# Optimization experiments

Measured on AMD Instinct MI355X. Metric: run time of the kernel, lower is better.

## Reference

```python
import jax, jax.numpy as jnp
import numpy as np

B, N, E, D = 1, 50000, 800000, 128


def _mlp(x, w1, b1, w2, b2, w3, b3):
    # MLP(in, hidden, out, l=2): Linear+ReLU, Linear+ReLU, Linear
    h = jax.nn.relu(x @ w1 + b1)
    h = jax.nn.relu(h @ w2 + b2)
    return h @ w3 + b3


def _glorot(key, shape):
    fan_in, fan_out = shape[0], shape[1]
    lim = np.sqrt(6.0 / (fan_in + fan_out)).astype(np.float32)
    return jax.random.uniform(key, shape, jnp.float32, -lim, lim)


def setup_inputs() -> dict:
    key = jax.random.key(0)
    ks = jax.random.split(key, 16)
    inp = {
        "nodes": jax.random.normal(ks[0], (B, N, D), jnp.float32),
        "senders": jax.random.randint(ks[1], (E,), 0, N, jnp.int32),
        "receivers": jax.random.randint(ks[2], (E,), 0, N, jnp.int32),
        # message MLP params: 2D -> D -> D -> D
        "mw1": _glorot(ks[3], (2 * D, D)), "mb1": jnp.zeros((D,), jnp.float32),
        "mw2": _glorot(ks[4], (D, D)),     "mb2": jnp.zeros((D,), jnp.float32),
        "mw3": _glorot(ks[5], (D, D)),     "mb3": jnp.zeros((D,), jnp.float32),
        # node MLP params: 2D -> D -> D -> D
        "nw1": _glorot(ks[6], (2 * D, D)), "nb1": jnp.zeros((D,), jnp.float32),
        "nw2": _glorot(ks[7], (D, D)),     "nb2": jnp.zeros((D,), jnp.float32),
        "nw3": _glorot(ks[8], (D, D)),     "nb3": jnp.zeros((D,), jnp.float32),
    }
    return inp


def reference(nodes, senders, receivers,
              mw1, mb1, mw2, mb2, mw3, mb3,
              nw1, nb1, nw2, nb2, nw3, nb3):
    # gather endpoint features: [B, E, 2D]
    edge_in = jnp.concatenate((nodes[:, receivers], nodes[:, senders]), axis=-1)
    messages = _mlp(edge_in, mw1, mb1, mw2, mb2, mw3, mb3)  # [B, E, D]
    # scatter-add messages into receiver inbox: [B, N, D]
    inbox = jnp.zeros_like(nodes).at[:, receivers].add(messages)
    node_in = jnp.concatenate((nodes, inbox), axis=-1)  # [B, N, 2D]
    return nodes + _mlp(node_in, nw1, nb1, nw2, nb2, nw3, nb3)
```

## Files before the change

### kernel.cpp

```cpp
#include <hip/hip_runtime.h>
#include <hip/hip_bf16.h>
#include <stdint.h>

typedef __bf16 bf16;
typedef bf16 bf16x8 __attribute__((ext_vector_type(8)));
typedef float f32x4 __attribute__((ext_vector_type(4)));

#define N_NODES 50000
#define FEAT 128
#define NB_SCAN ((N_NODES + 1023) / 1024)

static constexpr size_t UV_BYTES    = (size_t)N_NODES * 256 * 2;
static constexpr size_t INBOX_BYTES = (size_t)N_NODES * FEAT * 4;

#define WUV_OFF 0
#define WM2_OFF 32768
#define WM3_OFF 49152
#define WN1_OFF 65536
#define WN2_OFF 98304
#define WN3_OFF 114688
#define W_TOTAL 131072
static constexpr size_t W_BYTES = (size_t)W_TOTAL * 2;

__device__ __forceinline__ bf16x8 cvt_f32x8_bf16(const float* __restrict__ p) {
  float4 f0 = *(const float4*)p;
  float4 f1 = *(const float4*)(p + 4);
  bf16x8 t;
  t[0] = (bf16)f0.x; t[1] = (bf16)f0.y; t[2] = (bf16)f0.z; t[3] = (bf16)f0.w;
  t[4] = (bf16)f1.x; t[5] = (bf16)f1.y; t[6] = (bf16)f1.z; t[7] = (bf16)f1.w;
  return t;
}

__global__ void prep_weights_kernel(const float* __restrict__ mw1, const float* __restrict__ mw2,
                                    const float* __restrict__ mw3, const float* __restrict__ nw1,
                                    const float* __restrict__ nw2, const float* __restrict__ nw3,
                                    bf16* __restrict__ w) {
  int i = blockIdx.x * blockDim.x + threadIdx.x;
  if (i >= W_TOTAL) return;
  float v;
  if (i < WM2_OFF) {
    int c = i >> 7, k = i & 127;
    v = (c < 128) ? mw1[k * 128 + c] : mw1[(128 + k) * 128 + (c - 128)];
  } else if (i < WM3_OFF) {
    int j = i - WM2_OFF; int c = j >> 7, k = j & 127;
    v = mw2[k * 128 + c];
  } else if (i < WN1_OFF) {
    int j = i - WM3_OFF; int c = j >> 7, k = j & 127;
    v = mw3[k * 128 + c];
  } else if (i < WN2_OFF) {
    int j = i - WN1_OFF; int c = j >> 8, k = j & 255;
    v = nw1[k * 128 + c];
  } else if (i < WN3_OFF) {
    int j = i - WN2_OFF; int c = j >> 7, k = j & 127;
    v = nw2[k * 128 + c];
  } else {
    int j = i - WN3_OFF; int c = j >> 7, k = j & 127;
    v = nw3[k * 128 + c];
  }
  w[i] = (bf16)v;
}

__global__ void hist_kernel(const int* __restrict__ receivers, int* __restrict__ cnt, int E) {
  int i = blockIdx.x * blockDim.x + threadIdx.x;
  if (i < E) atomicAdd(&cnt[receivers[i]], 1);
}

__global__ __launch_bounds__(1024) void scan1_kernel(const int* __restrict__ cnt,
                                                     int* __restrict__ offs,
                                                     int* __restrict__ bsum) {
  __shared__ int s[1024];
  const int tid = threadIdx.x;
  const int g = blockIdx.x * 1024 + tid;
  int x = (g < N_NODES) ? cnt[g] : 0;
  s[tid] = x;
  __syncthreads();
  for (int off = 1; off < 1024; off <<= 1) {
    int v = (tid >= off) ? s[tid - off] : 0;
    __syncthreads();
    s[tid] += v;
    __syncthreads();
  }
  if (g < N_NODES) offs[g] = s[tid] - x;
  if (tid == 1023) bsum[blockIdx.x] = s[tid];
}

__global__ void scan2_kernel(int* __restrict__ bsum) {
  __shared__ int s[64];
  const int tid = threadIdx.x;
  int x = (tid < NB_SCAN) ? bsum[tid] : 0;
  s[tid] = x;
  __syncthreads();
  for (int off = 1; off < 64; off <<= 1) {
    int v = (tid >= off) ? s[tid - off] : 0;
    __syncthreads();
    s[tid] += v;
    __syncthreads();
  }
  if (tid < NB_SCAN) bsum[tid] = s[tid] - x;
}

__global__ __launch_bounds__(1024) void scan3_kernel(int* __restrict__ offs,
                                                     const int* __restrict__ bsum, int E) {
  const int tid = threadIdx.x;
  const int g = blockIdx.x * 1024 + tid;
  if (g < N_NODES) offs[g] += bsum[blockIdx.x];
  if (blockIdx.x == 0 && tid == 0) offs[N_NODES] = E;
}

__global__ void scatter_ids_kernel(const int* __restrict__ senders,
                                   const int* __restrict__ receivers,
                                   const int* __restrict__ offs, int* __restrict__ cur,
                                   int* __restrict__ sSend, int* __restrict__ sRecv, int E) {
  int i = blockIdx.x * blockDim.x + threadIdx.x;
  if (i < E) {
    int r = receivers[i];
    int slot = offs[r] + atomicAdd(&cur[r], 1);
    sSend[slot] = senders[i];
    sRecv[slot] = r;
  }
}

__global__ __launch_bounds__(512) void uv_gemm_kernel(const float* __restrict__ nodes,
                                                      const bf16* __restrict__ wuvt,
                                                      const float* __restrict__ mb1,
                                                      bf16* __restrict__ uv) {
  const int tid = threadIdx.x;
  const int lane = tid & 63, wid = tid >> 6;
  const int wm = wid >> 2, wn = wid & 3;
  const int rBase = blockIdx.x * 128 + wm * 64;
  const int cBase = wn * 64;
  const int l15 = lane & 15, ka = (lane >> 4) * 8, rj = (lane >> 4) * 4;

  f32x4 acc[4][4];
#pragma unroll
  for (int mi = 0; mi < 4; ++mi)
#pragma unroll
    for (int ni = 0; ni < 4; ++ni) acc[mi][ni] = (f32x4){0.f, 0.f, 0.f, 0.f};

#pragma unroll
  for (int kk = 0; kk < 4; ++kk) {
    const int k0 = kk * 32 + ka;
    bf16x8 a[4], b[4];
#pragma unroll
    for (int mi = 0; mi < 4; ++mi) {
      int r = rBase + mi * 16 + l15;
      if (r > N_NODES - 1) r = N_NODES - 1;
      a[mi] = cvt_f32x8_bf16(nodes + (size_t)r * FEAT + k0);
    }
#pragma unroll
    for (int ni = 0; ni < 4; ++ni) {
      int c = cBase + ni * 16 + l15;
      b[ni] = *(const bf16x8*)(wuvt + (size_t)c * 128 + k0);
    }
#pragma unroll
    for (int mi = 0; mi < 4; ++mi)
#pragma unroll
      for (int ni = 0; ni < 4; ++ni)
        acc[mi][ni] = __builtin_amdgcn_mfma_f32_16x16x32_bf16(a[mi], b[ni], acc[mi][ni], 0, 0, 0);
  }
#pragma unroll
  for (int mi = 0; mi < 4; ++mi)
#pragma unroll
    for (int ni = 0; ni < 4; ++ni) {
      int c = cBase + ni * 16 + l15;
      float bias = (c < FEAT) ? mb1[c] : 0.f;
#pragma unroll
      for (int j = 0; j < 4; ++j) {
        int r = rBase + mi * 16 + rj + j;
        if (r < N_NODES) uv[(size_t)r * 256 + c] = (bf16)(acc[mi][ni][j] + bias);
      }
    }
}

#define EB 128
__global__ __launch_bounds__(256, 3) void edge_kernel(const bf16* __restrict__ uv,
                                                      const int* __restrict__ sSend,
                                                      const int* __restrict__ sRecv,
                                                      const bf16* __restrict__ wm2t,
                                                      const bf16* __restrict__ wm3t,
                                                      const float* __restrict__ mb2,
                                                      const float* __restrict__ mb3,
                                                      float* __restrict__ inbox, int E) {
  __shared__ int rIds[EB];
  __shared__ int sIds[EB];
  __shared__ bf16 hbuf[4][32 * 128];

  const int tid = threadIdx.x;
  const int e0 = blockIdx.x * EB;
  const int rMax = (E - e0 < EB) ? (E - e0) : EB;

  if (tid < EB) {
    int e = e0 + tid; if (e >= E) e = E - 1;
    rIds[tid] = sRecv[e];
  } else {
    int t = tid - EB;
    int e = e0 + t; if (e >= E) e = E - 1;
    sIds[t] = sSend[e];
  }
  __syncthreads();

  const int lane = tid & 63, wid = tid >> 6;
  const int l15 = lane & 15, ka = (lane >> 4) * 8, rj = (lane >> 4) * 4;
  const int rW = wid * 32;
  bf16* hw = hbuf[wid];

  bf16x8 afr[2][4];
#pragma unroll
  for (int mi = 0; mi < 2; ++mi) {
    int row = rW + mi * 16 + l15;
    int recv = rIds[row], send = sIds[row];
    const bf16* up = uv + (size_t)recv * 256;
    const bf16* vp = uv + (size_t)send * 256 + 128;
#pragma unroll
    for (int kk = 0; kk < 4; ++kk) {
      int k0 = kk * 32 + ka;
      bf16x8 u8 = *(const bf16x8*)(up + k0);
      bf16x8 v8 = *(const bf16x8*)(vp + k0);
      bf16x8 h;
#pragma unroll
      for (int t = 0; t < 8; ++t) {
        float x = (float)u8[t] + (float)v8[t];
        h[t] = (bf16)(x > 0.f ? x : 0.f);
      }
      afr[mi][kk] = h;
    }
  }

  f32x4 acc[2][8];
#pragma unroll
  for (int mi = 0; mi < 2; ++mi)
#pragma unroll
    for (int ni = 0; ni < 8; ++ni) acc[mi][ni] = (f32x4){0.f, 0.f, 0.f, 0.f};
#pragma unroll
  for (int kk = 0; kk < 4; ++kk) {
    const int k0 = kk * 32 + ka;
    bf16x8 b[8];
#pragma unroll
    for (int ni = 0; ni < 8; ++ni) {
      int c = ni * 16 + l15;
      b[ni] = *(const bf16x8*)(wm2t + (size_t)c * 128 + k0);
    }
#pragma unroll
    for (int mi = 0; mi < 2; ++mi)
#pragma unroll
      for (int ni = 0; ni < 8; ++ni)
        acc[mi][ni] = __builtin_amdgcn_mfma_f32_16x16x32_bf16(afr[mi][kk], b[ni], acc[mi][ni], 0, 0, 0);
  }

#pragma unroll
  for (int mi = 0; mi < 2; ++mi)
#pragma unroll
    for (int ni = 0; ni < 8; ++ni) {
      int c = ni * 16 + l15;
      float bias = mb2[c];
#pragma unroll
      for (int j = 0; j < 4; ++j) {
        int row = mi * 16 + rj + j;
        float v = acc[mi][ni][j] + bias;
        v = v > 0.f ? v : 0.f;
        int byte = row * 256 + ((c * 2) ^ ((row & 7) << 4));
        *(bf16*)((char*)hw + byte) = (bf16)v;
      }
    }
  asm volatile("s_waitcnt lgkmcnt(0)" ::: "memory");
  __builtin_amdgcn_sched_barrier(0);

  bf16x8 a3[2][4];
#pragma unroll
  for (int mi = 0; mi < 2; ++mi) {
    int row = mi * 16 + l15;
#pragma unroll
    for (int kk = 0; kk < 4; ++kk) {
      int k0 = kk * 32 + ka;
      int byte = row * 256 + ((k0 * 2) ^ ((row & 7) << 4));
      a3[mi][kk] = *(const bf16x8*)((const char*)hw + byte);
    }
  }
  f32x4 acc3[2][8];
#pragma unroll
  for (int mi = 0; mi < 2; ++mi)
#pragma unroll
    for (int ni = 0; ni < 8; ++ni) acc3[mi][ni] = (f32x4){0.f, 0.f, 0.f, 0.f};
#pragma unroll
  for (int kk = 0; kk < 4; ++kk) {
    const int k0 = kk * 32 + ka;
    bf16x8 b[8];
#pragma unroll
    for (int ni = 0; ni < 8; ++ni) {
      int c = ni * 16 + l15;
      b[ni] = *(const bf16x8*)(wm3t + (size_t)c * 128 + k0);
    }
#pragma unroll
    for (int mi = 0; mi < 2; ++mi)
#pragma unroll
      for (int ni = 0; ni < 8; ++ni)
        acc3[mi][ni] = __builtin_amdgcn_mfma_f32_16x16x32_bf16(a3[mi][kk], b[ni], acc3[mi][ni], 0, 0, 0);
  }

  asm volatile("s_waitcnt lgkmcnt(0)" ::: "memory");
  __builtin_amdgcn_sched_barrier(0);
#pragma unroll
  for (int mi = 0; mi < 2; ++mi)
#pragma unroll
    for (int ni = 0; ni < 8; ++ni) {
      int c = ni * 16 + l15;
      float bias = mb3[c];
#pragma unroll
      for (int j = 0; j < 4; ++j) {
        int row = mi * 16 + rj + j;
        int byte = row * 256 + ((c * 2) ^ ((row & 7) << 4));
        *(bf16*)((char*)hw + byte) = (bf16)(acc3[mi][ni][j] + bias);
      }
    }
  asm volatile("s_waitcnt lgkmcnt(0)" ::: "memory");
  __builtin_amdgcn_sched_barrier(0);

  uint32_t pr[32];
#pragma unroll
  for (int r = 0; r < 32; ++r) {
    int byte = r * 256 + ((4 * lane) ^ ((r & 7) << 4));
    pr[r] = *(const uint32_t*)((const char*)hw + byte);
  }
  const int cb = 2 * lane;
  float s0 = 0.f, s1 = 0.f;
#pragma unroll
  for (int r = 0; r < 32; ++r) {
    int grow = rW + r;
    if (grow >= rMax) break;
    s0 += __uint_as_float(pr[r] << 16);
    s1 += __uint_as_float(pr[r] & 0xffff0000u);
    int recv = rIds[grow];
    bool flush = (r == 31) || (grow + 1 >= rMax) || (rIds[grow + 1] != recv);
    if (flush) {
      float* dst = inbox + (size_t)recv * FEAT + cb;
      unsafeAtomicAdd(dst, s0);
      unsafeAtomicAdd(dst + 1, s1);
      s0 = 0.f; s1 = 0.f;
    }
  }
}

__global__ __launch_bounds__(512) void node_kernel(const float* __restrict__ nodes,
                                                   const float* __restrict__ inbox,
                                                   const bf16* __restrict__ wn1t,
                                                   const bf16* __restrict__ wn2t,
                                                   const bf16* __restrict__ wn3t,
                                                   const float* __restrict__ nb1,
                                                   const float* __restrict__ nb2,
                                                   const float* __restrict__ nb3,
                                                   float* __restrict__ out) {
  __shared__ bf16 h1[256 * 128];
  __shared__ bf16 h2[256 * 128];
  const int tid = threadIdx.x;
  const int lane = tid & 63, wid = tid >> 6;
  const int wm = wid >> 1, wn = wid & 1;
  const int rBase = wm * 64, cBase = wn * 64;
  const int l15 = lane & 15, ka = (lane >> 4) * 8, rj = (lane >> 4) * 4;
  const int nBase = blockIdx.x * 256;

  f32x4 acc[4][4];
#pragma unroll
  for (int mi = 0; mi < 4; ++mi)
#pragma unroll
    for (int ni = 0; ni < 4; ++ni) acc[mi][ni] = (f32x4){0.f, 0.f, 0.f, 0.f};
#pragma unroll
  for (int kk = 0; kk < 8; ++kk) {
    const int k0 = kk * 32 + ka;
    bf16x8 a[4], b[4];
#pragma unroll
    for (int mi = 0; mi < 4; ++mi) {
      int n = nBase + rBase + mi * 16 + l15;
      if (n > N_NODES - 1) n = N_NODES - 1;
      const float* src = (kk < 4) ? (nodes + (size_t)n * FEAT + k0)
                                  : (inbox + (size_t)n * FEAT + (k0 - 128));
      a[mi] = cvt_f32x8_bf16(src);
    }
#pragma unroll
    for (int ni = 0; ni < 4; ++ni) {
      int c = cBase + ni * 16 + l15;
      b[ni] = *(const bf16x8*)(wn1t + (size_t)c * 256 + k0);
    }
#pragma unroll
    for (int mi = 0; mi < 4; ++mi)
#pragma unroll
      for (int ni = 0; ni < 4; ++ni)
        acc[mi][ni] = __builtin_amdgcn_mfma_f32_16x16x32_bf16(a[mi], b[ni], acc[mi][ni], 0, 0, 0);
  }
#pragma unroll
  for (int mi = 0; mi < 4; ++mi)
#pragma unroll
    for (int ni = 0; ni < 4; ++ni) {
      int c = cBase + ni * 16 + l15;
      float bias = nb1[c];
#pragma unroll
      for (int j = 0; j < 4; ++j) {
        int r = rBase + mi * 16 + rj + j;
        float v = acc[mi][ni][j] + bias;
        v = v > 0.f ? v : 0.f;
        int byte = r * 256 + ((c * 2) ^ ((r & 7) << 4));
        *(bf16*)((char*)h1 + byte) = (bf16)v;
      }
    }
  __syncthreads();

#pragma unroll
  for (int mi = 0; mi < 4; ++mi)
#pragma unroll
    for (int ni = 0; ni < 4; ++ni) acc[mi][ni] = (f32x4){0.f, 0.f, 0.f, 0.f};
#pragma unroll
  for (int kk = 0; kk < 4; ++kk) {
    const int k0 = kk * 32 + ka;
    bf16x8 a[4], b[4];
#pragma unroll
    for (int mi = 0; mi < 4; ++mi) {
      int r = rBase + mi * 16 + l15;
      int byte = r * 256 + ((k0 * 2) ^ ((r & 7) << 4));
      a[mi] = *(const bf16x8*)((const char*)h1 + byte);
    }
#pragma unroll
    for (int ni = 0; ni < 4; ++ni) {
      int c = cBase + ni * 16 + l15;
      b[ni] = *(const bf16x8*)(wn2t + (size_t)c * 128 + k0);
    }
#pragma unroll
    for (int mi = 0; mi < 4; ++mi)
#pragma unroll
      for (int ni = 0; ni < 4; ++ni)
        acc[mi][ni] = __builtin_amdgcn_mfma_f32_16x16x32_bf16(a[mi], b[ni], acc[mi][ni], 0, 0, 0);
  }
#pragma unroll
  for (int mi = 0; mi < 4; ++mi)
#pragma unroll
    for (int ni = 0; ni < 4; ++ni) {
      int c = cBase + ni * 16 + l15;
      float bias = nb2[c];
#pragma unroll
      for (int j = 0; j < 4; ++j) {
        int r = rBase + mi * 16 + rj + j;
        float v = acc[mi][ni][j] + bias;
        v = v > 0.f ? v : 0.f;
        int byte = r * 256 + ((c * 2) ^ ((r & 7) << 4));
        *(bf16*)((char*)h2 + byte) = (bf16)v;
      }
    }
  __syncthreads();

#pragma unroll
  for (int mi = 0; mi < 4; ++mi)
#pragma unroll
    for (int ni = 0; ni < 4; ++ni) acc[mi][ni] = (f32x4){0.f, 0.f, 0.f, 0.f};
#pragma unroll
  for (int kk = 0; kk < 4; ++kk) {
    const int k0 = kk * 32 + ka;
    bf16x8 a[4], b[4];
#pragma unroll
    for (int mi = 0; mi < 4; ++mi) {
      int r = rBase + mi * 16 + l15;
      int byte = r * 256 + ((k0 * 2) ^ ((r & 7) << 4));
      a[mi] = *(const bf16x8*)((const char*)h2 + byte);
    }
#pragma unroll
    for (int ni = 0; ni < 4; ++ni) {
      int c = cBase + ni * 16 + l15;
      b[ni] = *(const bf16x8*)(wn3t + (size_t)c * 128 + k0);
    }
#pragma unroll
    for (int mi = 0; mi < 4; ++mi)
#pragma unroll
      for (int ni = 0; ni < 4; ++ni)
        acc[mi][ni] = __builtin_amdgcn_mfma_f32_16x16x32_bf16(a[mi], b[ni], acc[mi][ni], 0, 0, 0);
  }
#pragma unroll
  for (int mi = 0; mi < 4; ++mi)
#pragma unroll
    for (int ni = 0; ni < 4; ++ni) {
      int c = cBase + ni * 16 + l15;
      float bias = nb3[c];
#pragma unroll
      for (int j = 0; j < 4; ++j) {
        int r = rBase + mi * 16 + rj + j;
        int n = nBase + r;
        if (n < N_NODES)
          out[(size_t)n * FEAT + c] = nodes[(size_t)n * FEAT + c] + acc[mi][ni][j] + bias;
      }
    }
}

extern "C" void kernel_launch(void* const* d_in, const int* in_sizes, int n_in,
                              void* d_out, int out_size, void* d_ws, size_t ws_size,
                              hipStream_t stream) {
  const float* nodes = (const float*)d_in[0];
  const int* senders = (const int*)d_in[1];
  const int* receivers = (const int*)d_in[2];
  const float* mw1 = (const float*)d_in[3];
  const float* mb1 = (const float*)d_in[4];
  const float* mw2 = (const float*)d_in[5];
  const float* mb2 = (const float*)d_in[6];
  const float* mw3 = (const float*)d_in[7];
  const float* mb3 = (const float*)d_in[8];
  const float* nw1 = (const float*)d_in[9];
  const float* nb1 = (const float*)d_in[10];
  const float* nw2 = (const float*)d_in[11];
  const float* nb2 = (const float*)d_in[12];
  const float* nw3 = (const float*)d_in[13];
  const float* nb3 = (const float*)d_in[14];
  float* out = (float*)d_out;
  const int E = in_sizes[1];

  char* ws = (char*)d_ws;
  bf16* uv = (bf16*)ws;
  bf16* w = (bf16*)(ws + UV_BYTES);
  char* p = ws + UV_BYTES + W_BYTES;
  float* inbox = (float*)p; p += INBOX_BYTES;
  int* offs = (int*)p; p += ((size_t)(N_NODES + 1) * 4 + 255) & ~255ull;
  int* cnt = (int*)p;  p += ((size_t)N_NODES * 4 + 255) & ~255ull;
  int* cur = (int*)p;  p += ((size_t)N_NODES * 4 + 255) & ~255ull;
  int* bsum = (int*)p; p += 256;
  int* sSend = (int*)p; p += ((size_t)E * 4 + 255) & ~255ull;
  int* sRecv = (int*)p; p += ((size_t)E * 4 + 255) & ~255ull;

  hipMemsetAsync(cnt, 0, (size_t)N_NODES * 4, stream);
  hipMemsetAsync(cur, 0, (size_t)N_NODES * 4, stream);
  hipMemsetAsync(inbox, 0, INBOX_BYTES, stream);
  prep_weights_kernel<<<(W_TOTAL + 255) / 256, 256, 0, stream>>>(mw1, mw2, mw3, nw1, nw2, nw3, w);
  hist_kernel<<<(E + 255) / 256, 256, 0, stream>>>(receivers, cnt, E);
  scan1_kernel<<<NB_SCAN, 1024, 0, stream>>>(cnt, offs, bsum);
  scan2_kernel<<<1, 64, 0, stream>>>(bsum);
  scan3_kernel<<<NB_SCAN, 1024, 0, stream>>>(offs, bsum, E);
  scatter_ids_kernel<<<(E + 255) / 256, 256, 0, stream>>>(senders, receivers, offs, cur,
                                                          sSend, sRecv, E);
  uv_gemm_kernel<<<(N_NODES + 127) / 128, 512, 0, stream>>>(nodes, w + WUV_OFF, mb1, uv);
  edge_kernel<<<(E + EB - 1) / EB, 256, 0, stream>>>(uv, sSend, sRecv, w + WM2_OFF, w + WM3_OFF,
                                                     mb2, mb3, inbox, E);
  node_kernel<<<(N_NODES + 255) / 256, 512, 0, stream>>>(nodes, inbox, w + WN1_OFF, w + WN2_OFF,
                                                         w + WN3_OFF, nb1, nb2, nb3, out);
}
```

Before: 476.9 us.

## Make edge kernel persistent with prefetched ids and register-level segmented reduction

```diff
diff --git a/kernel.cpp b/kernel.cpp
--- a/kernel.cpp
+++ b/kernel.cpp
@@ -9,6 +9,7 @@
 #define N_NODES 50000
 #define FEAT 128
 #define NB_SCAN ((N_NODES + 1023) / 1024)
+#define NBLK_EDGE 768
 
 static constexpr size_t UV_BYTES    = (size_t)N_NODES * 256 * 2;
 static constexpr size_t INBOX_BYTES = (size_t)N_NODES * FEAT * 4;
@@ -120,6 +121,17 @@
   }
 }
 
+__global__ void inbox_init_kernel(const int* __restrict__ cnt, const float* __restrict__ mb3,
+                                  float* __restrict__ inbox) {
+  int i = blockIdx.x * blockDim.x + threadIdx.x;
+  if (i >= N_NODES * 32) return;
+  int n = i >> 5, q = i & 31;
+  float c = (float)cnt[n];
+  float4 b = *(const float4*)(mb3 + q * 4);
+  float4 o = {c * b.x, c * b.y, c * b.z, c * b.w};
+  *(float4*)(inbox + (size_t)n * FEAT + q * 4) = o;
+}
+
 __global__ __launch_bounds__(512) void uv_gemm_kernel(const float* __restrict__ nodes,
                                                       const bf16* __restrict__ wuvt,
                                                       const float* __restrict__ mb1,
@@ -172,172 +184,199 @@
     }
 }
 
-#define EB 128
+__device__ __forceinline__ void seg_reduce(const f32x4 (&acc3)[2][8], int idr,
+                                           int lane, int l15, int rj,
+                                           float* __restrict__ inbox) {
+  int nxt = __shfl(idr, (lane & 31) + 1);
+  bool bnd = ((lane & 31) == 31) || (idr != nxt);
+  unsigned long long bm = __ballot(bnd);
+  uint32_t mask = (uint32_t)(bm & 0xffffffffull);
+  int lo = 0;
+  while (mask) {
+    int hi = __ffs(mask) - 1;
+    mask &= mask - 1;
+    int recv = __shfl(idr, hi);
+    if (recv >= 0) {
+      float s[8];
+#pragma unroll
+      for (int ni = 0; ni < 8; ++ni) {
+        float x = 0.f;
+#pragma unroll
+        for (int mi = 0; mi < 2; ++mi)
+#pragma unroll
+          for (int j = 0; j < 4; ++j) {
+            int row = mi * 16 + rj + j;
+            x += (row >= lo && row <= hi) ? acc3[mi][ni][j] : 0.f;
+          }
+        x += __shfl_xor(x, 16);
+        x += __shfl_xor(x, 32);
+        s[ni] = x;
+      }
+      if (lane < 16) {
+        float* dst = inbox + (size_t)recv * FEAT + l15;
+#pragma unroll
+        for (int ni = 0; ni < 8; ++ni) unsafeAtomicAdd(dst + ni * 16, s[ni]);
+      }
+    }
+    lo = hi + 1;
+  }
+}
+
 __global__ __launch_bounds__(256, 3) void edge_kernel(const bf16* __restrict__ uv,
                                                       const int* __restrict__ sSend,
                                                       const int* __restrict__ sRecv,
                                                       const bf16* __restrict__ wm2t,
                                                       const bf16* __restrict__ wm3t,
                                                       const float* __restrict__ mb2,
-                                                      const float* __restrict__ mb3,
                                                       float* __restrict__ inbox, int E) {
-  __shared__ int rIds[EB];
-  __shared__ int sIds[EB];
   __shared__ bf16 hbuf[4][32 * 128];
-
-  const int tid = threadIdx.x;
-  const int e0 = blockIdx.x * EB;
-  const int rMax = (E - e0 < EB) ? (E - e0) : EB;
-
-  if (tid < EB) {
-    int e = e0 + tid; if (e >= E) e = E - 1;
-    rIds[tid] = sRecv[e];
-  } else {
-    int t = tid - EB;
-    int e = e0 + t; if (e >= E) e = E - 1;
-    sIds[t] = sSend[e];
-  }
-  __syncthreads();
-
-  const int lane = tid & 63, wid = tid >> 6;
+  const int tid = threadIdx.x, lane = tid & 63, wid = tid >> 6;
   const int l15 = lane & 15, ka = (lane >> 4) * 8, rj = (lane >> 4) * 4;
-  const int rW = wid * 32;
+  const int l31 = lane & 31;
   bf16* hw = hbuf[wid];
-
-  bf16x8 afr[2][4];
-#pragma unroll
-  for (int mi = 0; mi < 2; ++mi) {
-    int row = rW + mi * 16 + l15;
-    int recv = rIds[row], send = sIds[row];
-    const bf16* up = uv + (size_t)recv * 256;
-    const bf16* vp = uv + (size_t)send * 256 + 128;
+  const int T = (E + 31) >> 5;
+  const int NW = NBLK_EDGE * 4;
+
+  float bias2[8];
+#pragma unroll
+  for (int ni = 0; ni < 8; ++ni) bias2[ni] = mb2[ni * 16 + l15];
+
+  f32x4 acc3[2][8];
+  int prevIdr = -1;
+  bool havePrev = false;
+
+  int t = blockIdx.x * 4 + wid;
+  int idr_c = -1, ids_c = 0;
+  if (t < T) {
+    int e = t * 32 + l31;
+    bool v = e < E;
+    int ec = v ? e : E - 1;
+    idr_c = v ? sRecv[ec] : -1;
+    ids_c = sSend[ec];
+  }
+
+  for (; t < T; t += NW) {
+    const int tn = t + NW;
+    int idr_n = -1, ids_n = 0;
+    if (tn < T) {
+      int e = tn * 32 + l31;
+      bool v = e < E;
+      int ec = v ? e : E - 1;
+      idr_n = v ? sRecv[ec] : -1;
+      ids_n = sSend[ec];
+    }
+
+    int rid[2], sid[2];
+#pragma unroll
+    for (int mi = 0; mi < 2; ++mi) {
+      int row = mi * 16 + l15;
+      int rv = __shfl(idr_c, row);
+      rid[mi] = rv < 0 ? 0 : rv;
+      sid[mi] = __shfl(ids_c, row);
+    }
+    bf16x8 U[2][4], V[2][4];
+#pragma unroll
+    for (int mi = 0; mi < 2; ++mi) {
+      const bf16* up = uv + (size_t)rid[mi] * 256;
+      const bf16* vp = uv + (size_t)sid[mi] * 256 + 128;
+#pragma unroll
+      for (int kk = 0; kk < 4; ++kk) {
+        U[mi][kk] = *(const bf16x8*)(up + kk * 32 + ka);
+        V[mi][kk] = *(const bf16x8*)(vp + kk * 32 + ka);
+      }
+    }
+
+    if (havePrev) seg_reduce(acc3, prevIdr, lane, l15, rj, inbox);
+
+    bf16x8 afr[2][4];
+#pragma unroll
+    for (int mi = 0; mi < 2; ++mi)
+#pragma unroll
+      for (int kk = 0; kk < 4; ++kk) {
+        bf16x8 h;
+#pragma unroll
+        for (int x = 0; x < 8; ++x) {
+          float s = (float)U[mi][kk][x] + (float)V[mi][kk][x];
+          h[x] = (bf16)(s > 0.f ? s : 0.f);
+        }
+        afr[mi][kk] = h;
+      }
+
+    f32x4 acc[2][8];
+#pragma unroll
+    for (int mi = 0; mi < 2; ++mi)
+#pragma unroll
+      for (int ni = 0; ni < 8; ++ni) acc[mi][ni] = (f32x4){0.f, 0.f, 0.f, 0.f};
 #pragma unroll
     for (int kk = 0; kk < 4; ++kk) {
-      int k0 = kk * 32 + ka;
-      bf16x8 u8 = *(const bf16x8*)(up + k0);
-      bf16x8 v8 = *(const bf16x8*)(vp + k0);
-      bf16x8 h;
-#pragma unroll
-      for (int t = 0; t < 8; ++t) {
-        float x = (float)u8[t] + (float)v8[t];
-        h[t] = (bf16)(x > 0.f ? x : 0.f);
-      }
-      afr[mi][kk] = h;
-    }
-  }
-
-  f32x4 acc[2][8];
-#pragma unroll
-  for (int mi = 0; mi < 2; ++mi)
-#pragma unroll
-    for (int ni = 0; ni < 8; ++ni) acc[mi][ni] = (f32x4){0.f, 0.f, 0.f, 0.f};
-#pragma unroll
-  for (int kk = 0; kk < 4; ++kk) {
-    const int k0 = kk * 32 + ka;
-    bf16x8 b[8];
-#pragma unroll
-    for (int ni = 0; ni < 8; ++ni) {
-      int c = ni * 16 + l15;
-      b[ni] = *(const bf16x8*)(wm2t + (size_t)c * 128 + k0);
-    }
+      const int k0 = kk * 32 + ka;
+      bf16x8 b[8];
+#pragma unroll
+      for (int ni = 0; ni < 8; ++ni) {
+        int c = ni * 16 + l15;
+        b[ni] = *(const bf16x8*)(wm2t + (size_t)c * 128 + k0);
+      }
+#pragma unroll
+      for (int mi = 0; mi < 2; ++mi)
+#pragma unroll
+        for (int ni = 0; ni < 8; ++ni)
+          acc[mi][ni] = __builtin_amdgcn_mfma_f32_16x16x32_bf16(afr[mi][kk], b[ni], acc[mi][ni], 0, 0, 0);
+    }
+
 #pragma unroll
     for (int mi = 0; mi < 2; ++mi)
 #pragma unroll
-      for (int ni = 0; ni < 8; ++ni)
-        acc[mi][ni] = __builtin_amdgcn_mfma_f32_16x16x32_bf16(afr[mi][kk], b[ni], acc[mi][ni], 0, 0, 0);
-  }
-
-#pragma unroll
-  for (int mi = 0; mi < 2; ++mi)
-#pragma unroll
-    for (int ni = 0; ni < 8; ++ni) {
-      int c = ni * 16 + l15;
-      float bias = mb2[c];
-#pragma unroll
-      for (int j = 0; j < 4; ++j) {
-        int row = mi * 16 + rj + j;
-        float v = acc[mi][ni][j] + bias;
-        v = v > 0.f ? v : 0.f;
-        int byte = row * 256 + ((c * 2) ^ ((row & 7) << 4));
-        *(bf16*)((char*)hw + byte) = (bf16)v;
-      }
-    }
-  asm volatile("s_waitcnt lgkmcnt(0)" ::: "memory");
-  __builtin_amdgcn_sched_barrier(0);
-
-  bf16x8 a3[2][4];
-#pragma unroll
-  for (int mi = 0; mi < 2; ++mi) {
-    int row = mi * 16 + l15;
+      for (int ni = 0; ni < 8; ++ni) {
+        int c = ni * 16 + l15;
+#pragma unroll
+        for (int j = 0; j < 4; ++j) {
+          int row = mi * 16 + rj + j;
+          float v = acc[mi][ni][j] + bias2[ni];
+          v = v > 0.f ? v : 0.f;
+          int byte = row * 256 + ((c * 2) ^ ((row & 7) << 4));
+          *(bf16*)((char*)hw + byte) = (bf16)v;
+        }
+      }
+    asm volatile("s_waitcnt lgkmcnt(0)" ::: "memory");
+    __builtin_amdgcn_sched_barrier(0);
+
+    bf16x8 a3[2][4];
+#pragma unroll
+    for (int mi = 0; mi < 2; ++mi) {
+      int row = mi * 16 + l15;
+#pragma unroll
+      for (int kk = 0; kk < 4; ++kk) {
+        int k0 = kk * 32 + ka;
+        int byte = row * 256 + ((k0 * 2) ^ ((row & 7) << 4));
+        a3[mi][kk] = *(const bf16x8*)((const char*)hw + byte);
+      }
+    }
+#pragma unroll
+    for (int mi = 0; mi < 2; ++mi)
+#pragma unroll
+      for (int ni = 0; ni < 8; ++ni) acc3[mi][ni] = (f32x4){0.f, 0.f, 0.f, 0.f};
 #pragma unroll
     for (int kk = 0; kk < 4; ++kk) {
-      int k0 = kk * 32 + ka;
-      int byte = row * 256 + ((k0 * 2) ^ ((row & 7) << 4));
-      a3[mi][kk] = *(const bf16x8*)((const char*)hw + byte);
-    }
-  }
-  f32x4 acc3[2][8];
-#pragma unroll
-  for (int mi = 0; mi < 2; ++mi)
-#pragma unroll
-    for (int ni = 0; ni < 8; ++ni) acc3[mi][ni] = (f32x4){0.f, 0.f, 0.f, 0.f};
-#pragma unroll
-  for (int kk = 0; kk < 4; ++kk) {
-    const int k0 = kk * 32 + ka;
-    bf16x8 b[8];
-#pragma unroll
-    for (int ni = 0; ni < 8; ++ni) {
-      int c = ni * 16 + l15;
-      b[ni] = *(const bf16x8*)(wm3t + (size_t)c * 128 + k0);
-    }
-#pragma unroll
-    for (int mi = 0; mi < 2; ++mi)
-#pragma unroll
-      for (int ni = 0; ni < 8; ++ni)
-        acc3[mi][ni] = __builtin_amdgcn_mfma_f32_16x16x32_bf16(a3[mi][kk], b[ni], acc3[mi][ni], 0, 0, 0);
-  }
-
-  asm volatile("s_waitcnt lgkmcnt(0)" ::: "memory");
-  __builtin_amdgcn_sched_barrier(0);
-#pragma unroll
-  for (int mi = 0; mi < 2; ++mi)
-#pragma unroll
-    for (int ni = 0; ni < 8; ++ni) {
-      int c = ni * 16 + l15;
-      float bias = mb3[c];
-#pragma unroll
-      for (int j = 0; j < 4; ++j) {
-        int row = mi * 16 + rj + j;
-        int byte = row * 256 + ((c * 2) ^ ((row & 7) << 4));
-        *(bf16*)((char*)hw + byte) = (bf16)(acc3[mi][ni][j] + bias);
-      }
-    }
-  asm volatile("s_waitcnt lgkmcnt(0)" ::: "memory");
-  __builtin_amdgcn_sched_barrier(0);
-
-  uint32_t pr[32];
-#pragma unroll
-  for (int r = 0; r < 32; ++r) {
-    int byte = r * 256 + ((4 * lane) ^ ((r & 7) << 4));
-    pr[r] = *(const uint32_t*)((const char*)hw + byte);
-  }
-  const int cb = 2 * lane;
-  float s0 = 0.f, s1 = 0.f;
-#pragma unroll
-  for (int r = 0; r < 32; ++r) {
-    int grow = rW + r;
-    if (grow >= rMax) break;
-    s0 += __uint_as_float(pr[r] << 16);
-    s1 += __uint_as_float(pr[r] & 0xffff0000u);
-    int recv = rIds[grow];
-    bool flush = (r == 31) || (grow + 1 >= rMax) || (rIds[grow + 1] != recv);
-    if (flush) {
-      float* dst = inbox + (size_t)recv * FEAT + cb;
-      unsafeAtomicAdd(dst, s0);
-      unsafeAtomicAdd(dst + 1, s1);
-      s0 = 0.f; s1 = 0.f;
-    }
-  }
+      const int k0 = kk * 32 + ka;
+      bf16x8 b[8];
+#pragma unroll
+      for (int ni = 0; ni < 8; ++ni) {
+        int c = ni * 16 + l15;
+        b[ni] = *(const bf16x8*)(wm3t + (size_t)c * 128 + k0);
+      }
+#pragma unroll
+      for (int mi = 0; mi < 2; ++mi)
+#pragma unroll
+        for (int ni = 0; ni < 8; ++ni)
+          acc3[mi][ni] = __builtin_amdgcn_mfma_f32_16x16x32_bf16(a3[mi][kk], b[ni], acc3[mi][ni], 0, 0, 0);
+    }
+
+    prevIdr = idr_c;
+    havePrev = true;
+    idr_c = idr_n;
+    ids_c = ids_n;
+  }
+  if (havePrev) seg_reduce(acc3, prevIdr, lane, l15, rj, inbox);
 }
 
 __global__ __launch_bounds__(512) void node_kernel(const float* __restrict__ nodes,
@@ -521,7 +560,6 @@
 
   hipMemsetAsync(cnt, 0, (size_t)N_NODES * 4, stream);
   hipMemsetAsync(cur, 0, (size_t)N_NODES * 4, stream);
-  hipMemsetAsync(inbox, 0, INBOX_BYTES, stream);
   prep_weights_kernel<<<(W_TOTAL + 255) / 256, 256, 0, stream>>>(mw1, mw2, mw3, nw1, nw2, nw3, w);
   hist_kernel<<<(E + 255) / 256, 256, 0, stream>>>(receivers, cnt, E);
   scan1_kernel<<<NB_SCAN, 1024, 0, stream>>>(cnt, offs, bsum);
@@ -529,9 +567,10 @@
   scan3_kernel<<<NB_SCAN, 1024, 0, stream>>>(offs, bsum, E);
   scatter_ids_kernel<<<(E + 255) / 256, 256, 0, stream>>>(senders, receivers, offs, cur,
                                                           sSend, sRecv, E);
+  inbox_init_kernel<<<(N_NODES * 32 + 255) / 256, 256, 0, stream>>>(cnt, mb3, inbox);
   uv_gemm_kernel<<<(N_NODES + 127) / 128, 512, 0, stream>>>(nodes, w + WUV_OFF, mb1, uv);
-  edge_kernel<<<(E + EB - 1) / EB, 256, 0, stream>>>(uv, sSend, sRecv, w + WM2_OFF, w + WM3_OFF,
-                                                     mb2, mb3, inbox, E);
+  edge_kernel<<<NBLK_EDGE, 256, 0, stream>>>(uv, sSend, sRecv, w + WM2_OFF, w + WM3_OFF,
+                                             mb2, inbox, E);
   node_kernel<<<(N_NODES + 255) / 256, 512, 0, stream>>>(nodes, inbox, w + WN1_OFF, w + WN2_OFF,
                                                          w + WN3_OFF, nb1, nb2, nb3, out);
 }
```

Result: slower. 714.7 us (+49.9%).
